# Kernel optimization log

Measured on AMD Instinct MI355X. Metric: run time of the kernel, lower is better.

Reference implementation:

```python
import jax, jax.numpy as jnp
import numpy as np


def _unfold(x, k):
    # x: [B, C, H, W] -> [B, C, S, L] with S=k*k (row-major patch order), L=H*W
    B, C, H, W = x.shape
    pad = k // 2
    xp = jnp.pad(x, ((0, 0), (0, 0), (pad, pad), (pad, pad)))
    patches = jnp.stack(
        [xp[:, :, r:r + H, c:c + W] for r in range(k) for c in range(k)], axis=2
    )  # [B, C, S, H, W]
    return patches.reshape(B, C, k * k, H * W)


def setup_inputs() -> dict:
    key = jax.random.key(0)
    ks = jax.random.split(key, 8)
    B, C, H, W = 8, 64, 128, 128
    R, Cout = 4, 128
    x = jax.random.normal(ks[0], (B, C, H, W), dtype=jnp.float32)
    gate_w = jax.random.normal(ks[1], (R, C), dtype=jnp.float32) * 0.05   # 1x1 gate conv weight
    gate_b = jax.random.normal(ks[2], (R,), dtype=jnp.float32) * 0.01
    theta = jax.random.normal(ks[3], (R,), dtype=jnp.float32) * 0.5       # learned directions
    raw_sigma_u = jax.random.normal(ks[4], (R,), dtype=jnp.float32) * 0.1
    raw_sigma_s = jax.random.normal(ks[5], (R,), dtype=jnp.float32) * 0.1
    pw_w = jax.random.normal(ks[6], (Cout, R * C), dtype=jnp.float32) * (1.0 / np.sqrt(R * C).astype(np.float32))
    pw_b = jax.random.normal(ks[7], (Cout,), dtype=jnp.float32) * 0.01
    return {"x": x, "gate_w": gate_w, "gate_b": gate_b, "theta": theta,
            "raw_sigma_u": raw_sigma_u, "raw_sigma_s": raw_sigma_s,
            "pw_w": pw_w, "pw_b": pw_b}


def reference(x, gate_w, gate_b, theta, raw_sigma_u, raw_sigma_s, pw_w, pw_b):
    k = 3
    B, C, H, W = x.shape
    R = theta.shape[0]
    S, L = k * k, H * W

    x_un = _unfold(x, k)                                         # [B, C, S, L]

    # 1x1 gate conv + fuzzy softmax over rules
    logits = jnp.einsum('bchw,rc->brhw', x, gate_w) + gate_b[None, :, None, None]
    mu = jax.nn.softmax(logits, axis=1)                          # [B, R, H, W]
    mu_un = _unfold(mu, k)                                       # [B, R, S, L]
    s_center = (k // 2) * k + (k // 2)
    mu_center = mu_un[:, :, s_center:s_center + 1, :]            # [B, R, 1, L]

    # anisotropic Gaussian kernel per rule over integer offsets (row-major)
    grid = np.arange(k, dtype=np.float32) - k // 2
    dy = jnp.asarray(np.repeat(grid, k))                         # [S]
    dx = jnp.asarray(np.tile(grid, k))                           # [S]
    cos_t, sin_t = jnp.cos(theta)[:, None], jnp.sin(theta)[:, None]
    proj_u = cos_t * dx[None, :] + sin_t * dy[None, :]           # [R, S]
    proj_s = -sin_t * dx[None, :] + cos_t * dy[None, :]
    su = (jax.nn.softplus(raw_sigma_u) + 1e-4)[:, None]
    ss = (jax.nn.softplus(raw_sigma_s) + 1e-4)[:, None]
    kern = jnp.exp(-proj_u ** 2 / su ** 2 - proj_s ** 2 / ss ** 2)  # [R, S]

    alpha = mu_center * mu_un * kern[None, :, :, None]           # [B, R, S, L]
    alpha_sum = jnp.maximum(alpha.sum(axis=(1, 2), keepdims=True), 1e-8)
    alpha = alpha / alpha_sum

    agg = jnp.einsum('brsl,bcsl->brcl', alpha, x_un)             # [B, R, C, L]
    agg_flat = agg.reshape(B, R * C, L)
    out = jnp.einsum('bnl,on->bol', agg_flat, pw_w) + pw_b[None, :, None]
    return out.reshape(B, -1, H, W)
```

## Files before the change

### kernel.cpp

```cpp
#include <hip/hip_runtime.h>
#include <math.h>

#define CC 64
#define RR 4
#define HH 128
#define WW 128
#define BB 8
#define COUT 128
#define XCH 164
#define ALS 44

typedef __attribute__((ext_vector_type(8))) short short8;
typedef __attribute__((ext_vector_type(4))) float f32x4;
typedef __attribute__((ext_vector_type(2))) float f32x2;

__device__ __forceinline__ unsigned short f2bf(float f) {
  unsigned u = __float_as_uint(f);
  u += 0x7fffu + ((u >> 16) & 1u);
  return (unsigned short)(u >> 16);
}
__device__ __forceinline__ float bf2f(unsigned short h) {
  return __uint_as_float(((unsigned)h) << 16);
}

__global__ __launch_bounds__(256) void k_pre(const float* __restrict__ theta,
                                             const float* __restrict__ rsu,
                                             const float* __restrict__ rss,
                                             const float* __restrict__ pw,
                                             const float* __restrict__ gw,
                                             float* __restrict__ wkern,
                                             unsigned short* __restrict__ pwb,
                                             unsigned short* __restrict__ gwb) {
  int i = blockIdx.x * 256 + threadIdx.x;
  if (i < COUT * RR * CC) pwb[i] = f2bf(pw[i]);
  if (blockIdx.x == 0 && threadIdx.x < RR * 9) {
    int t = threadIdx.x;
    int r = t / 9, s = t % 9;
    float dy = (float)(s / 3 - 1), dx = (float)(s % 3 - 1);
    float ct = cosf(theta[r]), st = sinf(theta[r]);
    float su = log1pf(expf(rsu[r])) + 1e-4f;
    float sv = log1pf(expf(rss[r])) + 1e-4f;
    float pu = ct * dx + st * dy;
    float ps = -st * dx + ct * dy;
    wkern[t] = expf(-(pu * pu) / (su * su) - (ps * ps) / (sv * sv));
  }
  if (blockIdx.x == 1) {
    #pragma unroll
    for (int k = 0; k < 4; ++k) {
      int j = k * 256 + threadIdx.x;
      gwb[j] = (j < RR * CC) ? f2bf(gw[j]) : (unsigned short)0;
    }
  }
}

__global__ __launch_bounds__(256, 3) void k_fused(const float* __restrict__ x,
                                                  const float* __restrict__ gwb_unused,
                                                  const float* __restrict__ gb,
                                                  const float* __restrict__ wkern,
                                                  const unsigned short* __restrict__ pwb,
                                                  const unsigned short* __restrict__ gwb,
                                                  const float* __restrict__ pb,
                                                  float* __restrict__ out) {
  __shared__ unsigned short xs[CC][XCH];
  __shared__ float mus[RR][4][40];
  __shared__ unsigned short alp[64][ALS];
  __shared__ float rsum[RR][64];
  __shared__ __align__(16) unsigned short aggs[16][264];

  int tid = threadIdx.x;
  int raw = blockIdx.x;
  int bid = (raw & 7) * 256 + (raw >> 3);
  int b = bid >> 8;
  int rem = bid & 255;
  int h0 = (rem >> 2) << 1;
  int w0 = (rem & 3) << 5;

  int lane = tid & 63;
  int wv = tid >> 6;
  int lr = lane & 15, lq = lane >> 4;
  int o0 = wv << 5;

  short8 a0r[8], a1r[8];
  {
    const unsigned short* pA = pwb + ((o0 + lr) << 8) + (lq << 3);
    #pragma unroll
    for (int ks = 0; ks < 8; ++ks) {
      a0r[ks] = *(const short8*)(pA + (ks << 5));
      a1r[ks] = *(const short8*)(pA + 4096 + (ks << 5));
    }
  }
  short8 am0 = *(const short8*)(gwb + (lr << 6) + (lq << 3));
  short8 am1 = *(const short8*)(gwb + (lr << 6) + 32 + (lq << 3));
  float4 pbv0 = *(const float4*)&pb[o0 + (lq << 2)];
  float4 pbv1 = *(const float4*)&pb[o0 + 16 + (lq << 2)];
  float gb0 = gb[0], gb1 = gb[1], gb2 = gb[2], gb3 = gb[3];

  #pragma unroll
  for (int k = 0; k < 10; ++k) {
    unsigned idx = (unsigned)(k * 256 + tid);
    unsigned c4 = idx % 10u;
    unsigned pair = idx / 10u;
    int c = pair >> 2, row = pair & 3;
    int gcol = w0 - 4 + (c4 << 2);
    int grow = h0 - 1 + row;
    float4 v = make_float4(0.f, 0.f, 0.f, 0.f);
    if ((unsigned)gcol < WW && (unsigned)grow < HH)
      v = *(const float4*)(x + (((size_t)b * CC + c) << 14) + (grow << 7) + gcol);
    ushort4 uv;
    uv.x = f2bf(v.x); uv.y = f2bf(v.y); uv.z = f2bf(v.z); uv.w = f2bf(v.w);
    *(ushort4*)&xs[c][row * 40 + (c4 << 2)] = uv;
  }
  __syncthreads();

  for (int j = wv; j < 9; j += 4) {
    int p = (j << 4) + lr;
    int pcl = p > 135 ? 135 : p;
    unsigned y = (unsigned)pcl / 34u;
    int cxo = pcl - (int)(y * 34u);
    int pos = (int)y * 40 + 3 + cxo;
    short8 b0, b1;
    #pragma unroll
    for (int i = 0; i < 8; ++i) {
      b0[i] = (short)xs[(lq << 3) + i][pos];
      b1[i] = (short)xs[32 + (lq << 3) + i][pos];
    }
    f32x4 mac = (f32x4){0.f, 0.f, 0.f, 0.f};
    mac = __builtin_amdgcn_mfma_f32_16x16x32_bf16(am0, b0, mac, 0, 0, 0);
    mac = __builtin_amdgcn_mfma_f32_16x16x32_bf16(am1, b1, mac, 0, 0, 0);
    if (lq == 0 && p < 136) {
      int grow = h0 - 1 + (int)y, gcol = w0 - 1 + cxo;
      float lg0 = mac[0] + gb0, lg1 = mac[1] + gb1;
      float lg2 = mac[2] + gb2, lg3 = mac[3] + gb3;
      float m = fmaxf(fmaxf(lg0, lg1), fmaxf(lg2, lg3));
      float e0 = expf(lg0 - m), e1 = expf(lg1 - m);
      float e2 = expf(lg2 - m), e3 = expf(lg3 - m);
      float inv = 1.0f / (e0 + e1 + e2 + e3);
      if (!((unsigned)grow < HH && (unsigned)gcol < WW)) inv = 0.0f;
      mus[0][y][3 + cxo] = e0 * inv;
      mus[1][y][3 + cxo] = e1 * inv;
      mus[2][y][3 + cxo] = e2 * inv;
      mus[3][y][3 + cxo] = e3 * inv;
    }
  }
  __syncthreads();

  {
    int t = tid & 63, r = tid >> 6;
    int prow = t >> 5, pcol = t & 31;
    float mc = mus[r][prow + 1][pcol + 4];
    float sum = 0.f;
    #pragma unroll
    for (int s = 0; s < 9; ++s) {
      float av = mc * mus[r][prow + s / 3][pcol + 3 + s % 3] * wkern[r * 9 + s];
      alp[t][(s << 2) + r] = f2bf(av);
      sum += av;
    }
    rsum[r][t] = sum;
  }
  __syncthreads();

  f32x4 dprev0 = (f32x4){0.f, 0.f, 0.f, 0.f};
  f32x4 dprev1 = (f32x4){0.f, 0.f, 0.f, 0.f};
  #pragma unroll
  for (int rd = 0; rd < 4; ++rd) {
    {
      int t16 = tid & 15, cg = tid >> 4, c0 = cg << 2;
      int px = (rd << 4) + t16;
      int prow2 = px >> 5, pc = px & 31;
      float inv = 1.0f / fmaxf(rsum[0][px] + rsum[1][px] + rsum[2][px] + rsum[3][px], 1e-8f);

      uint2 ad[9];
      #pragma unroll
      for (int s = 0; s < 9; ++s) ad[s] = *(const uint2*)(&alp[px][s << 2]);

      f32x2 cacc[4][2];
      #pragma unroll
      for (int r = 0; r < 4; ++r) {
        cacc[r][0] = (f32x2){0.f, 0.f};
        cacc[r][1] = (f32x2){0.f, 0.f};
      }

      f32x2 xv[2][2];
      {
        int xo = prow2 * 40 + pc + 3;
        xv[0][0][0] = bf2f(xs[c0][xo]);     xv[0][0][1] = bf2f(xs[c0 + 1][xo]);
        xv[0][1][0] = bf2f(xs[c0 + 2][xo]); xv[0][1][1] = bf2f(xs[c0 + 3][xo]);
      }
      #pragma unroll
      for (int s = 0; s < 9; ++s) {
        if (s < 8) {
          int sn = s + 1;
          int xo = (prow2 + sn / 3) * 40 + pc + 3 + sn % 3;
          xv[(s + 1) & 1][0][0] = bf2f(xs[c0][xo]);
          xv[(s + 1) & 1][0][1] = bf2f(xs[c0 + 1][xo]);
          xv[(s + 1) & 1][1][0] = bf2f(xs[c0 + 2][xo]);
          xv[(s + 1) & 1][1][1] = bf2f(xs[c0 + 3][xo]);
        }
        unsigned adx = ad[s].x, ady = ad[s].y;
        float af0 = __uint_as_float(adx << 16);
        float af1 = __uint_as_float(adx & 0xffff0000u);
        float af2 = __uint_as_float(ady << 16);
        float af3 = __uint_as_float(ady & 0xffff0000u);
        f32x2 A0 = {af0, af0}, A1 = {af1, af1}, A2 = {af2, af2}, A3 = {af3, af3};
        f32x2 x0 = xv[s & 1][0], x1 = xv[s & 1][1];
        cacc[0][0] += A0 * x0; cacc[0][1] += A0 * x1;
        cacc[1][0] += A1 * x0; cacc[1][1] += A1 * x1;
        cacc[2][0] += A2 * x0; cacc[2][1] += A2 * x1;
        cacc[3][0] += A3 * x0; cacc[3][1] += A3 * x1;
      }
      #pragma unroll
      for (int r = 0; r < 4; ++r) {
        ushort4 wvv;
        wvv.x = f2bf(cacc[r][0][0] * inv); wvv.y = f2bf(cacc[r][0][1] * inv);
        wvv.z = f2bf(cacc[r][1][0] * inv); wvv.w = f2bf(cacc[r][1][1] * inv);
        *(ushort4*)&aggs[t16][(r << 6) + c0] = wvv;
      }
    }
    __syncthreads();

    {
      f32x4 dacc0 = (f32x4){0.f, 0.f, 0.f, 0.f};
      f32x4 dacc1 = (f32x4){0.f, 0.f, 0.f, 0.f};
      #pragma unroll
      for (int ks = 0; ks < 8; ++ks) {
        short8 b0 = *(const short8*)&aggs[lr][(ks << 5) + (lq << 3)];
        dacc0 = __builtin_amdgcn_mfma_f32_16x16x32_bf16(a0r[ks], b0, dacc0, 0, 0, 0);
        dacc1 = __builtin_amdgcn_mfma_f32_16x16x32_bf16(a1r[ks], b0, dacc1, 0, 0, 0);
      }
      if ((rd & 1) == 0) {
        dprev0 = dacc0; dprev1 = dacc1;
      } else {
        int orow = h0 + (rd >> 1);
        #pragma unroll
        for (int q = 0; q < 4; ++q) {
          int o = o0 + (lq << 2) + q;
          size_t base0 = (((size_t)b * COUT + o) << 14) + (orow << 7) + w0;
          size_t base1 = (((size_t)b * COUT + o + 16) << 14) + (orow << 7) + w0;
          out[base0 + lr]      = dprev0[q] + pbv0[q];
          out[base0 + 16 + lr] = dacc0[q] + pbv0[q];
          out[base1 + lr]      = dprev1[q] + pbv1[q];
          out[base1 + 16 + lr] = dacc1[q] + pbv1[q];
        }
      }
    }
    if (rd < 3) __syncthreads();
  }
}

extern "C" void kernel_launch(void* const* d_in, const int* in_sizes, int n_in,
                              void* d_out, int out_size, void* d_ws, size_t ws_size,
                              hipStream_t stream) {
  const float* x     = (const float*)d_in[0];
  const float* gw    = (const float*)d_in[1];
  const float* gb    = (const float*)d_in[2];
  const float* theta = (const float*)d_in[3];
  const float* rsu   = (const float*)d_in[4];
  const float* rss   = (const float*)d_in[5];
  const float* pw    = (const float*)d_in[6];
  const float* pb    = (const float*)d_in[7];
  float* outp = (float*)d_out;

  float* wkern = (float*)d_ws;
  unsigned short* pwb = (unsigned short*)(wkern + 64);
  unsigned short* gwb = pwb + COUT * RR * CC;

  k_pre<<<128, 256, 0, stream>>>(theta, rsu, rss, pw, gw, wkern, pwb, gwb);
  k_fused<<<BB * (HH / 2) * (WW / 32), 256, 0, stream>>>(x, nullptr, gb, wkern,
                                                         pwb, gwb, pb, outp);
}
```

Measured before the change: 60.24 us.

## Transpose LDS x tile to spatial-major and process a full row per round

Stores the bf16 x tile transposed as [position][channel], so MFMA B operands and the aggregation reads become single 8/16-byte vector LDS loads instead of eight scalar loads. The aggregation stage now handles 32 pixels × 8 channels per thread in two rounds instead of four, with doubled MFMA work per round and half the barriers. In exchange, the tile is written with scalar 2-byte transposed stores that may cause bank conflicts, and per-thread register pressure rises.

Result: no change. 59.26 us (-1.6%).

```diff
diff --git a/kernel.cpp b/kernel.cpp
--- a/kernel.cpp
+++ b/kernel.cpp
@@ -7,7 +7,7 @@
 #define WW 128
 #define BB 8
 #define COUT 128
-#define XCH 164
+#define XST 72
 #define ALS 44
 
 typedef __attribute__((ext_vector_type(8))) short short8;
@@ -22,6 +22,8 @@
 __device__ __forceinline__ float bf2f(unsigned short h) {
   return __uint_as_float(((unsigned)h) << 16);
 }
+__device__ __forceinline__ float blo(unsigned u) { return __uint_as_float(u << 16); }
+__device__ __forceinline__ float bhi(unsigned u) { return __uint_as_float(u & 0xffff0000u); }
 
 __global__ __launch_bounds__(256) void k_pre(const float* __restrict__ theta,
                                              const float* __restrict__ rsu,
@@ -54,18 +56,17 @@
 }
 
 __global__ __launch_bounds__(256, 3) void k_fused(const float* __restrict__ x,
-                                                  const float* __restrict__ gwb_unused,
                                                   const float* __restrict__ gb,
                                                   const float* __restrict__ wkern,
                                                   const unsigned short* __restrict__ pwb,
                                                   const unsigned short* __restrict__ gwb,
                                                   const float* __restrict__ pb,
                                                   float* __restrict__ out) {
-  __shared__ unsigned short xs[CC][XCH];
+  __shared__ unsigned short xsT[160][XST];
   __shared__ float mus[RR][4][40];
   __shared__ unsigned short alp[64][ALS];
   __shared__ float rsum[RR][64];
-  __shared__ __align__(16) unsigned short aggs[16][264];
+  __shared__ __align__(16) unsigned short aggs[32][264];
 
   int tid = threadIdx.x;
   int raw = blockIdx.x;
@@ -106,9 +107,11 @@
     float4 v = make_float4(0.f, 0.f, 0.f, 0.f);
     if ((unsigned)gcol < WW && (unsigned)grow < HH)
       v = *(const float4*)(x + (((size_t)b * CC + c) << 14) + (grow << 7) + gcol);
-    ushort4 uv;
-    uv.x = f2bf(v.x); uv.y = f2bf(v.y); uv.z = f2bf(v.z); uv.w = f2bf(v.w);
-    *(ushort4*)&xs[c][row * 40 + (c4 << 2)] = uv;
+    int sp = row * 40 + (c4 << 2);
+    xsT[sp][c]     = f2bf(v.x);
+    xsT[sp + 1][c] = f2bf(v.y);
+    xsT[sp + 2][c] = f2bf(v.z);
+    xsT[sp + 3][c] = f2bf(v.w);
   }
   __syncthreads();
 
@@ -118,12 +121,8 @@
     unsigned y = (unsigned)pcl / 34u;
     int cxo = pcl - (int)(y * 34u);
     int pos = (int)y * 40 + 3 + cxo;
-    short8 b0, b1;
-    #pragma unroll
-    for (int i = 0; i < 8; ++i) {
-      b0[i] = (short)xs[(lq << 3) + i][pos];
-      b1[i] = (short)xs[32 + (lq << 3) + i][pos];
-    }
+    short8 b0 = *(const short8*)&xsT[pos][lq << 3];
+    short8 b1 = *(const short8*)&xsT[pos][32 + (lq << 3)];
     f32x4 mac = (f32x4){0.f, 0.f, 0.f, 0.f};
     mac = __builtin_amdgcn_mfma_f32_16x16x32_bf16(am0, b0, mac, 0, 0, 0);
     mac = __builtin_amdgcn_mfma_f32_16x16x32_bf16(am1, b1, mac, 0, 0, 0);
@@ -159,91 +158,79 @@
   }
   __syncthreads();
 
-  f32x4 dprev0 = (f32x4){0.f, 0.f, 0.f, 0.f};
-  f32x4 dprev1 = (f32x4){0.f, 0.f, 0.f, 0.f};
   #pragma unroll
-  for (int rd = 0; rd < 4; ++rd) {
+  for (int p = 0; p < 2; ++p) {
     {
-      int t16 = tid & 15, cg = tid >> 4, c0 = cg << 2;
-      int px = (rd << 4) + t16;
-      int prow2 = px >> 5, pc = px & 31;
+      int t = tid & 31, cg = tid >> 5, c0 = cg << 3;
+      int px = (p << 5) + t;
       float inv = 1.0f / fmaxf(rsum[0][px] + rsum[1][px] + rsum[2][px] + rsum[3][px], 1e-8f);
 
       uint2 ad[9];
       #pragma unroll
       for (int s = 0; s < 9; ++s) ad[s] = *(const uint2*)(&alp[px][s << 2]);
 
-      f32x2 cacc[4][2];
+      f32x2 cacc[4][4];
+      #pragma unroll
+      for (int r = 0; r < 4; ++r)
+        #pragma unroll
+        for (int j = 0; j < 4; ++j) cacc[r][j] = (f32x2){0.f, 0.f};
+
+      #pragma unroll
+      for (int s = 0; s < 9; ++s) {
+        uint4 ux = *(const uint4*)&xsT[(p + s / 3) * 40 + t + 3 + s % 3][c0];
+        f32x2 xv0 = {blo(ux.x), bhi(ux.x)};
+        f32x2 xv1 = {blo(ux.y), bhi(ux.y)};
+        f32x2 xv2 = {blo(ux.z), bhi(ux.z)};
+        f32x2 xv3 = {blo(ux.w), bhi(ux.w)};
+        unsigned adx = ad[s].x, ady = ad[s].y;
+        float af0 = blo(adx), af1 = bhi(adx), af2 = blo(ady), af3 = bhi(ady);
+        f32x2 A0 = {af0, af0}, A1 = {af1, af1}, A2 = {af2, af2}, A3 = {af3, af3};
+        cacc[0][0] += A0 * xv0; cacc[0][1] += A0 * xv1; cacc[0][2] += A0 * xv2; cacc[0][3] += A0 * xv3;
+        cacc[1][0] += A1 * xv0; cacc[1][1] += A1 * xv1; cacc[1][2] += A1 * xv2; cacc[1][3] += A1 * xv3;
+        cacc[2][0] += A2 * xv0; cacc[2][1] += A2 * xv1; cacc[2][2] += A2 * xv2; cacc[2][3] += A2 * xv3;
+        cacc[3][0] += A3 * xv0; cacc[3][1] += A3 * xv1; cacc[3][2] += A3 * xv2; cacc[3][3] += A3 * xv3;
+      }
       #pragma unroll
       for (int r = 0; r < 4; ++r) {
-        cacc[r][0] = (f32x2){0.f, 0.f};
-        cacc[r][1] = (f32x2){0.f, 0.f};
+        short8 wvv;
+        #pragma unroll
+        for (int j = 0; j < 4; ++j) {
+          wvv[2 * j]     = (short)f2bf(cacc[r][j][0] * inv);
+          wvv[2 * j + 1] = (short)f2bf(cacc[r][j][1] * inv);
+        }
+        *(short8*)&aggs[t][(r << 6) + c0] = wvv;
       }
-
-      f32x2 xv[2][2];
-      {
-        int xo = prow2 * 40 + pc + 3;
-        xv[0][0][0] = bf2f(xs[c0][xo]);     xv[0][0][1] = bf2f(xs[c0 + 1][xo]);
-        xv[0][1][0] = bf2f(xs[c0 + 2][xo]); xv[0][1][1] = bf2f(xs[c0 + 3][xo]);
+    }
+    __syncthreads();
+
+    f32x4 dacc[2][2];
+    #pragma unroll
+    for (int i = 0; i < 2; ++i)
+      #pragma unroll
+      for (int j = 0; j < 2; ++j) dacc[i][j] = (f32x4){0.f, 0.f, 0.f, 0.f};
+
+    #pragma unroll
+    for (int ks = 0; ks < 8; ++ks) {
+      short8 b0 = *(const short8*)&aggs[lr][(ks << 5) + (lq << 3)];
+      short8 b1 = *(const short8*)&aggs[16 + lr][(ks << 5) + (lq << 3)];
+      dacc[0][0] = __builtin_amdgcn_mfma_f32_16x16x32_bf16(a0r[ks], b0, dacc[0][0], 0, 0, 0);
+      dacc[0][1] = __builtin_amdgcn_mfma_f32_16x16x32_bf16(a0r[ks], b1, dacc[0][1], 0, 0, 0);
+      dacc[1][0] = __builtin_amdgcn_mfma_f32_16x16x32_bf16(a1r[ks], b0, dacc[1][0], 0, 0, 0);
+      dacc[1][1] = __builtin_amdgcn_mfma_f32_16x16x32_bf16(a1r[ks], b1, dacc[1][1], 0, 0, 0);
+    }
+
+    #pragma unroll
+    for (int oi = 0; oi < 2; ++oi) {
+      float4 pbv = oi ? pbv1 : pbv0;
+      #pragma unroll
+      for (int q = 0; q < 4; ++q) {
+        int o = o0 + (oi << 4) + (lq << 2) + q;
+        size_t base = (((size_t)b * COUT + o) << 14) + ((h0 + p) << 7) + w0;
+        out[base + lr]      = dacc[oi][0][q] + pbv[q];
+        out[base + 16 + lr] = dacc[oi][1][q] + pbv[q];
       }
-      #pragma unroll
-      for (int s = 0; s < 9; ++s) {
-        if (s < 8) {
-          int sn = s + 1;
-          int xo = (prow2 + sn / 3) * 40 + pc + 3 + sn % 3;
-          xv[(s + 1) & 1][0][0] = bf2f(xs[c0][xo]);
-          xv[(s + 1) & 1][0][1] = bf2f(xs[c0 + 1][xo]);
-          xv[(s + 1) & 1][1][0] = bf2f(xs[c0 + 2][xo]);
-          xv[(s + 1) & 1][1][1] = bf2f(xs[c0 + 3][xo]);
-        }
-        unsigned adx = ad[s].x, ady = ad[s].y;
-        float af0 = __uint_as_float(adx << 16);
-        float af1 = __uint_as_float(adx & 0xffff0000u);
-        float af2 = __uint_as_float(ady << 16);
-        float af3 = __uint_as_float(ady & 0xffff0000u);
-        f32x2 A0 = {af0, af0}, A1 = {af1, af1}, A2 = {af2, af2}, A3 = {af3, af3};
-        f32x2 x0 = xv[s & 1][0], x1 = xv[s & 1][1];
-        cacc[0][0] += A0 * x0; cacc[0][1] += A0 * x1;
-        cacc[1][0] += A1 * x0; cacc[1][1] += A1 * x1;
-        cacc[2][0] += A2 * x0; cacc[2][1] += A2 * x1;
-        cacc[3][0] += A3 * x0; cacc[3][1] += A3 * x1;
-      }
-      #pragma unroll
-      for (int r = 0; r < 4; ++r) {
-        ushort4 wvv;
-        wvv.x = f2bf(cacc[r][0][0] * inv); wvv.y = f2bf(cacc[r][0][1] * inv);
-        wvv.z = f2bf(cacc[r][1][0] * inv); wvv.w = f2bf(cacc[r][1][1] * inv);
-        *(ushort4*)&aggs[t16][(r << 6) + c0] = wvv;
-      }
-    }
-    __syncthreads();
-
-    {
-      f32x4 dacc0 = (f32x4){0.f, 0.f, 0.f, 0.f};
-      f32x4 dacc1 = (f32x4){0.f, 0.f, 0.f, 0.f};
-      #pragma unroll
-      for (int ks = 0; ks < 8; ++ks) {
-        short8 b0 = *(const short8*)&aggs[lr][(ks << 5) + (lq << 3)];
-        dacc0 = __builtin_amdgcn_mfma_f32_16x16x32_bf16(a0r[ks], b0, dacc0, 0, 0, 0);
-        dacc1 = __builtin_amdgcn_mfma_f32_16x16x32_bf16(a1r[ks], b0, dacc1, 0, 0, 0);
-      }
-      if ((rd & 1) == 0) {
-        dprev0 = dacc0; dprev1 = dacc1;
-      } else {
-        int orow = h0 + (rd >> 1);
-        #pragma unroll
-        for (int q = 0; q < 4; ++q) {
-          int o = o0 + (lq << 2) + q;
-          size_t base0 = (((size_t)b * COUT + o) << 14) + (orow << 7) + w0;
-          size_t base1 = (((size_t)b * COUT + o + 16) << 14) + (orow << 7) + w0;
-          out[base0 + lr]      = dprev0[q] + pbv0[q];
-          out[base0 + 16 + lr] = dacc0[q] + pbv0[q];
-          out[base1 + lr]      = dprev1[q] + pbv1[q];
-          out[base1 + 16 + lr] = dacc1[q] + pbv1[q];
-        }
-      }
-    }
-    if (rd < 3) __syncthreads();
+    }
+    if (p == 0) __syncthreads();
   }
 }
 
@@ -265,6 +252,5 @@
   unsigned short* gwb = pwb + COUT * RR * CC;
 
   k_pre<<<128, 256, 0, stream>>>(theta, rsu, rss, pw, gw, wkern, pwb, gwb);
-  k_fused<<<BB * (HH / 2) * (WW / 32), 256, 0, stream>>>(x, nullptr, gb, wkern,
-                                                         pwb, gwb, pb, outp);
-}
+  k_fused<<<BB * (HH / 2) * (WW / 32), 256, 0, stream>>>(x, gb, wkern, pwb, gwb, pb, outp);
+}
```
